# Performance work log

Measured on AMD Instinct MI355X. Metric: run time of the kernel, lower is better.

## Reference

```python
import jax, jax.numpy as jnp
import numpy as np

W_KERNEL = 5      # dilation kernel size (w)
K_BG = 0.1        # background weight (k)
RELAX = 5.0       # sigmoid temperature (relax)
INF = 1e4         # 'no zero in column' sentinel (>> image diagonal)
EPS = 1e-7        # DiceLoss eps


def setup_inputs() -> dict:
    key = jax.random.key(0)
    k1, k2 = jax.random.split(key)
    B, H, W = 32, 256, 256
    preds = jax.random.normal(k1, (B, H, W), dtype=jnp.float32)
    targets = (jax.random.uniform(k2, (B, H, W)) > 0.99).astype(jnp.float32)
    return {"preds": preds, "targets": targets}


def _dilate(t, w):
    # cv2.dilate with w x w ones kernel == sliding-window max, SAME padding
    pad = w // 2
    return jax.lax.reduce_window(t, -jnp.inf, jax.lax.max,
                                 (1, w, w), (1, 1, 1),
                                 [(0, 0), (pad, pad), (pad, pad)])


def _vertical_dist(zero_mask):
    # per-column distance (in rows) to nearest zero pixel; [B,H,W] -> [B,H,W]
    B, H, W = zero_mask.shape
    rows = jnp.moveaxis(zero_mask, 1, 0)  # [H,B,W]

    def step(carry, z):
        d = jnp.where(z, 0.0, jnp.minimum(carry + 1.0, INF))
        return d, d

    init = jnp.full((B, W), INF, dtype=jnp.float32)
    _, fwd = jax.lax.scan(step, init, rows)
    _, bwd = jax.lax.scan(step, init, rows[::-1])
    g = jnp.minimum(fwd, bwd[::-1])  # [H,B,W]
    return jnp.moveaxis(g, 0, 1)


def _edt(fat):
    # exact euclidean distance transform (distance to nearest zero pixel),
    # separable two-pass: vertical 1D distance, then horizontal min-plus.
    B, H, W = fat.shape
    g = _vertical_dist(fat == 0)  # [B,H,W]
    col = jnp.arange(W, dtype=jnp.float32)
    off2 = (col[:, None] - col[None, :]) ** 2  # [W_j, W_k]

    def per_img(gi):  # gi: [H,W]
        # d2[i,j] = min_k g[i,k]^2 + (j-k)^2   -> [H,W,W] intermediate
        d2 = jnp.min(gi[:, None, :] ** 2 + off2[None, :, :], axis=-1)
        return jnp.sqrt(d2)

    return jax.lax.map(per_img, g)  # sequential over batch caps memory


def _distance_maps(targets):
    fat = _dilate(targets, W_KERNEL)          # [B,H,W]
    d = _edt(fat)                              # [B,H,W]
    soft = jax.nn.sigmoid(d / RELAX)
    soft = soft - jnp.min(soft, axis=(1, 2), keepdims=True)
    mx = jnp.max(soft, axis=(1, 2), keepdims=True)
    soft = soft / jnp.where(mx > 0, mx, 1.0)
    dm_soft = soft + (1.0 - fat) * K_BG
    has_fg = jnp.max(targets, axis=(1, 2), keepdims=True) > 0
    return jnp.where(has_fg, dm_soft, 1.0 - targets)


def reference(preds, targets):
    p = jax.nn.sigmoid(preds)
    dm = jax.lax.stop_gradient(_distance_maps(targets))  # computed in numpy in torch => constant
    pw = p * dm
    bs = pw.shape[0]
    y_pred = pw.reshape(bs, 1, -1)
    y_true = targets.reshape(bs, 1, -1)
    # smp DiceLoss('binary', from_logits=False): dims=(0,2), smooth=0, eps=1e-7
    inter = jnp.sum(y_pred * y_true, axis=(0, 2))
    card = jnp.sum(y_pred + y_true, axis=(0, 2))
    dice = (2.0 * inter) / jnp.maximum(card, EPS)
    loss = 1.0 - dice
    mask = (jnp.sum(y_true, axis=(0, 2)) > 0).astype(loss.dtype)
    return jnp.mean(loss * mask)
```

## Files before the change

kernel.cpp:

```cpp
#include <hip/hip_runtime.h>
#include <math.h>

#define BB 32
#define HH 256
#define WW 256
#define HW (HH*WW)
#define K_BG 0.1f
#define RELAX 5.0f
#define EPS_D 1e-7
#define RPB 8

typedef unsigned long long u64;
typedef unsigned short u16;

__device__ __forceinline__ float sigf(float x) { return 1.0f / (1.0f + expf(-x)); }

__device__ __forceinline__ u64 shflx64(u64 x, int s) {
    return (u64)__shfl_xor((unsigned long long)x, s, 64);
}

__global__ void k_maskdil(const float* __restrict__ tg, u64* __restrict__ dmaskT,
                          u64* __restrict__ nzmask) {
    __shared__ u64 nz[20][4];
    __shared__ u64 hd[20][4];
    int blk = blockIdx.x;
    int b = blk >> 4, band = blk & 15;
    int r0 = band * 16;
    int t = threadIdx.x, w = t >> 6;
    const float* img = tg + b * HW;
    float v[20];
    #pragma unroll
    for (int rr = 0; rr < 20; ++rr) {
        int rg = r0 + rr - 2;
        v[rr] = (rg >= 0 && rg < HH) ? img[rg * WW + t] : 0.0f;
    }
    #pragma unroll
    for (int rr = 0; rr < 20; ++rr) {
        u64 bal = __ballot(v[rr] != 0.0f);
        if ((t & 63) == 0) nz[rr][w] = bal;
    }
    __syncthreads();
    if (t < 80) {
        int rr = t >> 2, k = t & 3;
        u64 m = nz[rr][k];
        u64 ml = (k > 0) ? nz[rr][k - 1] : 0ULL;
        u64 mr = (k < 3) ? nz[rr][k + 1] : 0ULL;
        hd[rr][k] = m | (m << 1) | (m << 2) | (m >> 1) | (m >> 2)
                  | (ml >> 62) | (ml >> 63) | (mr << 62) | (mr << 63);
    }
    if (t < 64) {
        int rr = t >> 2, k = t & 3;
        nzmask[b * 1024 + (r0 + rr) * 4 + k] = nz[rr + 2][k];
    }
    __syncthreads();
    if (t < 64) {
        int rr = t >> 2, k = t & 3;
        u64 o = hd[rr][k] | hd[rr + 1][k] | hd[rr + 2][k] | hd[rr + 3][k] | hd[rr + 4][k];
        dmaskT[b * 1024 + k * 256 + (r0 + rr)] = o;
    }
}

__global__ void k_transp(const u64* __restrict__ dmaskT, u64* __restrict__ cmask) {
    int b = blockIdx.x;
    int tid = threadIdx.x, lane = tid & 63, wv = tid >> 6;
    const u64* base = dmaskT + b * 1024;
    const u64 L32 = 0x00000000FFFFFFFFULL, L16 = 0x0000FFFF0000FFFFULL,
              L8  = 0x00FF00FF00FF00FFULL, L4  = 0x0F0F0F0F0F0F0F0FULL,
              L2  = 0x3333333333333333ULL, L1  = 0x5555555555555555ULL;
    #pragma unroll
    for (int w = 0; w < 4; ++w) {
        u64 x = base[w * 256 + wv * 64 + lane];
        u64 pp;
        pp = shflx64(x, 32); x = (lane & 32) ? ((x & ~L32) | ((pp & ~L32) >> 32)) : ((x & L32) | ((pp & L32) << 32));
        pp = shflx64(x, 16); x = (lane & 16) ? ((x & ~L16) | ((pp & ~L16) >> 16)) : ((x & L16) | ((pp & L16) << 16));
        pp = shflx64(x,  8); x = (lane &  8) ? ((x & ~L8 ) | ((pp & ~L8 ) >>  8)) : ((x & L8 ) | ((pp & L8 ) <<  8));
        pp = shflx64(x,  4); x = (lane &  4) ? ((x & ~L4 ) | ((pp & ~L4 ) >>  4)) : ((x & L4 ) | ((pp & L4 ) <<  4));
        pp = shflx64(x,  2); x = (lane &  2) ? ((x & ~L2 ) | ((pp & ~L2 ) >>  2)) : ((x & L2 ) | ((pp & L2 ) <<  2));
        pp = shflx64(x,  1); x = (lane &  1) ? ((x & ~L1 ) | ((pp & ~L1 ) >>  1)) : ((x & L1 ) | ((pp & L1 ) <<  1));
        cmask[b * 1024 + (w * 64 + lane) * 4 + wv] = x;
    }
}

__global__ __launch_bounds__(256) void k_mega(const float* __restrict__ preds,
                                              const u64* __restrict__ cmask,
                                              const u64* __restrict__ nzmask,
                                              float4* __restrict__ part1,
                                              float4* __restrict__ part2) {
    __shared__ u16 gS[RPB][WW];
    __shared__ float red[8][4];
    int blk = blockIdx.x;
    int b = blk >> 5, q = blk & 31;
    int i0 = q * RPB;
    int tid = threadIdx.x;
    int lane = tid & 63, wv = tid >> 6;
    int j = tid;

    float p[RPB];
    #pragma unroll
    for (int rr = 0; rr < RPB; ++rr)
        p[rr] = preds[(b * HH + i0 + rr) * WW + j];
    u64 nzw[RPB];
    #pragma unroll
    for (int rr = 0; rr < RPB; ++rr)
        nzw[rr] = nzmask[b * 1024 + (i0 + rr) * 4 + wv];

    u64 yw[4];
    {
        const u64* cm = cmask + b * 1024 + j * 4;
        #pragma unroll
        for (int g = 0; g < 4; ++g) yw[g] = ~cm[g];
    }

    int g0v[RPB], fgv[RPB];
    #pragma unroll
    for (int rr = 0; rr < RPB; ++rr) {
        int i = i0 + rr;
        int iw = i >> 6, ib = i & 63;
        u64 lowm  = (2ULL << ib) - 1ULL;
        u64 highm = ~((1ULL << ib) - 1ULL);
        int pu = -1, pd = -1;
        #pragma unroll
        for (int w = 0; w < 4; ++w) {
            u64 m = (w < iw) ? ~0ULL : ((w == iw) ? lowm : 0ULL);
            u64 z = yw[w] & m;
            int cand = (w << 6) + 63 - __clzll(z);
            pu = z ? cand : pu;
        }
        #pragma unroll
        for (int w = 3; w >= 0; --w) {
            u64 m = (w > iw) ? ~0ULL : ((w == iw) ? highm : 0ULL);
            u64 z = yw[w] & m;
            int cand = (w << 6) + (__ffsll((unsigned long long)z) - 1);
            pd = z ? cand : pd;
        }
        int up = (pu >= 0) ? (i - pu) : 10000;
        int dn = (pd >= 0) ? (pd - i) : 10000;
        int g0 = min(min(up, dn), 10000);
        g0v[rr] = g0;
        fgv[rr] = (int)((~yw[iw] >> ib) & 1ULL);
        gS[rr][j] = (u16)g0;
    }
    __syncthreads();

    float vals[8];
    #pragma unroll
    for (int qq = 0; qq < 6; ++qq) vals[qq] = 0.0f;
    vals[6] = 1e30f; vals[7] = 0.0f;
    #pragma unroll
    for (int rr = 0; rr < RPB; ++rr) {
        float gv = (float)g0v[rr];
        float best = gv * gv;
        #pragma unroll
        for (int r = 1; r <= 8; ++r) {
            float rf = (float)(r * r);
            int jl = j - r, jr = j + r;
            float vl = (jl >= 0) ? (float)gS[rr][jl] : 1e4f;
            float vr = (jr < WW) ? (float)gS[rr][jr] : 1e4f;
            best = fminf(best, fminf(fmaf(vl, vl, rf), fmaf(vr, vr, rf)));
        }
        for (int r = 9; r < WW; ++r) {
            float rf = (float)(r * r);
            if (rf >= best) break;
            int jl = j - r, jr = j + r;
            if (jl >= 0) { float v = (float)gS[rr][jl]; best = fminf(best, fmaf(v, v, rf)); }
            if (jr < WW) { float v = (float)gS[rr][jr]; best = fminf(best, fmaf(v, v, rf)); }
        }
        float dv = sqrtf(best);
        float sp = sigf(p[rr]);
        float sd = sigf(dv / RELAX);
        float tv = (float)((nzw[rr] >> (j & 63)) & 1ULL);
        vals[0] += sp * sd * tv;
        vals[1] += sp * tv;
        vals[2] += sp * sd;
        vals[3] += sp;
        vals[4] += fgv[rr] ? 0.0f : sp;
        vals[5] += tv;
        vals[6] = fminf(vals[6], dv);
        vals[7] = fmaxf(vals[7], dv);
    }
    for (int off = 32; off > 0; off >>= 1) {
        #pragma unroll
        for (int qq = 0; qq < 6; ++qq) vals[qq] += __shfl_down(vals[qq], off, 64);
        vals[6] = fminf(vals[6], __shfl_down(vals[6], off, 64));
        vals[7] = fmaxf(vals[7], __shfl_down(vals[7], off, 64));
    }
    if (lane == 0) {
        #pragma unroll
        for (int qq = 0; qq < 8; ++qq) red[qq][wv] = vals[qq];
    }
    __syncthreads();
    if (tid == 0) {
        float s[8];
        #pragma unroll
        for (int qq = 0; qq < 6; ++qq) s[qq] = red[qq][0] + red[qq][1] + red[qq][2] + red[qq][3];
        s[6] = fminf(fminf(red[6][0], red[6][1]), fminf(red[6][2], red[6][3]));
        s[7] = fmaxf(fmaxf(red[7][0], red[7][1]), fmaxf(red[7][2], red[7][3]));
        part1[blk] = make_float4(s[0], s[1], s[2], s[3]);
        part2[blk] = make_float4(s[4], s[5], s[6], s[7]);
    }
}

__global__ void k_tail(const float4* __restrict__ part1, const float4* __restrict__ part2,
                       float* __restrict__ out) {
    __shared__ float sI[32], sC[32], sA[32];
    int t = threadIdx.x;
    #pragma unroll
    for (int pass = 0; pass < 4; ++pass) {
        int img = pass * 8 + (t >> 5);
        int k = t & 31;
        float4 p1 = part1[img * 32 + k];
        float4 p2 = part2[img * 32 + k];
        float vals[8] = {p1.x, p1.y, p1.z, p1.w, p2.x, p2.y, p2.z, p2.w};
        for (int off = 16; off > 0; off >>= 1) {
            #pragma unroll
            for (int qq = 0; qq < 6; ++qq) vals[qq] += __shfl_down(vals[qq], off, 32);
            vals[6] = fminf(vals[6], __shfl_down(vals[6], off, 32));
            vals[7] = fmaxf(vals[7], __shfl_down(vals[7], off, 32));
        }
        if (k == 0) {
            float A = vals[0], Bs = vals[1], Ap = vals[2], Bp = vals[3];
            float Cp = vals[4], T = vals[5], dmn = vals[6], dmx = vals[7];
            float inter, card, any;
            if (dmx > 0.0f) {
                float smin = sigf(dmn / RELAX);
                float smax = sigf(dmx / RELAX);
                float m = smax - smin;
                float denom = (m > 0.0f) ? m : 1.0f;
                inter = (A - smin * Bs) / denom;
                card  = (Ap - smin * Bp) / denom + K_BG * Cp + T;
                any = 1.0f;
            } else {
                inter = 0.0f;
                card = Bp - Bs + T;
                any = 0.0f;
            }
            sI[img] = inter; sC[img] = card; sA[img] = any;
        }
    }
    __syncthreads();
    if (t == 0) {
        double I = 0.0, C = 0.0;
        int any = 0;
        for (int b = 0; b < BB; ++b) {
            I += (double)sI[b]; C += (double)sC[b];
            any |= (sA[b] > 0.0f);
        }
        double dice = 2.0 * I / fmax(C, (double)EPS_D);
        out[0] = any ? (float)(1.0 - dice) : 0.0f;
    }
}

extern "C" void kernel_launch(void* const* d_in, const int* in_sizes, int n_in,
                              void* d_out, int out_size, void* d_ws, size_t ws_size,
                              hipStream_t stream) {
    const float* preds = (const float*)d_in[0];
    const float* tg    = (const float*)d_in[1];
    float* out = (float*)d_out;

    u64* dmaskT   = (u64*)d_ws;
    u64* nzmask   = dmaskT + BB * 1024;
    u64* cmask    = nzmask + BB * 1024;
    float4* part1 = (float4*)(cmask + BB * 1024);
    float4* part2 = part1 + BB * 32;

    hipLaunchKernelGGL(k_maskdil, dim3(BB * 16), dim3(WW), 0, stream, tg, dmaskT, nzmask);
    hipLaunchKernelGGL(k_transp, dim3(BB), dim3(WW), 0, stream, dmaskT, cmask);
    hipLaunchKernelGGL(k_mega, dim3(BB * 32), dim3(WW), 0, stream, preds, cmask, nzmask,
                       part1, part2);
    hipLaunchKernelGGL(k_tail, dim3(1), dim3(256), 0, stream, part1, part2, out);
}
```

Before: 93.02 us.

## Fuse bit-transpose into main kernel and unroll horizontal EDT search by 8

```diff
diff --git a/kernel.cpp b/kernel.cpp
--- a/kernel.cpp
+++ b/kernel.cpp
@@ -60,9 +60,30 @@
     }
 }
 
-__global__ void k_transp(const u64* __restrict__ dmaskT, u64* __restrict__ cmask) {
-    int b = blockIdx.x;
-    int tid = threadIdx.x, lane = tid & 63, wv = tid >> 6;
+__global__ __launch_bounds__(256) void k_mega(const float* __restrict__ preds,
+                                              const u64* __restrict__ dmaskT,
+                                              const u64* __restrict__ nzmask,
+                                              float4* __restrict__ part1,
+                                              float4* __restrict__ part2) {
+    __shared__ u64 colT[4 * 256];
+    __shared__ u16 gS[RPB][WW];
+    __shared__ float red[8][4];
+    int blk = blockIdx.x;
+    int b = blk >> 5, q = blk & 31;
+    int i0 = q * RPB;
+    int tid = threadIdx.x;
+    int lane = tid & 63, wv = tid >> 6;
+    int j = tid;
+
+    float p[RPB];
+    #pragma unroll
+    for (int rr = 0; rr < RPB; ++rr)
+        p[rr] = preds[(b * HH + i0 + rr) * WW + j];
+    u64 nzw[RPB];
+    #pragma unroll
+    for (int rr = 0; rr < RPB; ++rr)
+        nzw[rr] = nzmask[b * 1024 + (i0 + rr) * 4 + wv];
+
     const u64* base = dmaskT + b * 1024;
     const u64 L32 = 0x00000000FFFFFFFFULL, L16 = 0x0000FFFF0000FFFFULL,
               L8  = 0x00FF00FF00FF00FFULL, L4  = 0x0F0F0F0F0F0F0F0FULL,
@@ -77,39 +98,13 @@
         pp = shflx64(x,  4); x = (lane &  4) ? ((x & ~L4 ) | ((pp & ~L4 ) >>  4)) : ((x & L4 ) | ((pp & L4 ) <<  4));
         pp = shflx64(x,  2); x = (lane &  2) ? ((x & ~L2 ) | ((pp & ~L2 ) >>  2)) : ((x & L2 ) | ((pp & L2 ) <<  2));
         pp = shflx64(x,  1); x = (lane &  1) ? ((x & ~L1 ) | ((pp & ~L1 ) >>  1)) : ((x & L1 ) | ((pp & L1 ) <<  1));
-        cmask[b * 1024 + (w * 64 + lane) * 4 + wv] = x;
-    }
-}
-
-__global__ __launch_bounds__(256) void k_mega(const float* __restrict__ preds,
-                                              const u64* __restrict__ cmask,
-                                              const u64* __restrict__ nzmask,
-                                              float4* __restrict__ part1,
-                                              float4* __restrict__ part2) {
-    __shared__ u16 gS[RPB][WW];
-    __shared__ float red[8][4];
-    int blk = blockIdx.x;
-    int b = blk >> 5, q = blk & 31;
-    int i0 = q * RPB;
-    int tid = threadIdx.x;
-    int lane = tid & 63, wv = tid >> 6;
-    int j = tid;
-
-    float p[RPB];
-    #pragma unroll
-    for (int rr = 0; rr < RPB; ++rr)
-        p[rr] = preds[(b * HH + i0 + rr) * WW + j];
-    u64 nzw[RPB];
-    #pragma unroll
-    for (int rr = 0; rr < RPB; ++rr)
-        nzw[rr] = nzmask[b * 1024 + (i0 + rr) * 4 + wv];
+        colT[wv * 256 + w * 64 + lane] = x;
+    }
+    __syncthreads();
 
     u64 yw[4];
-    {
-        const u64* cm = cmask + b * 1024 + j * 4;
-        #pragma unroll
-        for (int g = 0; g < 4; ++g) yw[g] = ~cm[g];
-    }
+    #pragma unroll
+    for (int g = 0; g < 4; ++g) yw[g] = ~colT[g * 256 + j];
 
     int g0v[RPB], fgv[RPB];
     #pragma unroll
@@ -158,12 +153,17 @@
             float vr = (jr < WW) ? (float)gS[rr][jr] : 1e4f;
             best = fminf(best, fminf(fmaf(vl, vl, rf), fmaf(vr, vr, rf)));
         }
-        for (int r = 9; r < WW; ++r) {
-            float rf = (float)(r * r);
-            if (rf >= best) break;
-            int jl = j - r, jr = j + r;
-            if (jl >= 0) { float v = (float)gS[rr][jl]; best = fminf(best, fmaf(v, v, rf)); }
-            if (jr < WW) { float v = (float)gS[rr][jr]; best = fminf(best, fmaf(v, v, rf)); }
+        for (int rc = 9; rc < WW + 8; rc += 8) {
+            if ((float)(rc * rc) >= best) break;
+            #pragma unroll
+            for (int dr = 0; dr < 8; ++dr) {
+                int r = rc + dr;
+                float rf = (float)(r * r);
+                int jl = j - r, jr = j + r;
+                float vl = (jl >= 0) ? (float)gS[rr][jl] : 1e4f;
+                float vr = (jr < WW) ? (float)gS[rr][jr] : 1e4f;
+                best = fminf(best, fminf(fmaf(vl, vl, rf), fmaf(vr, vr, rf)));
+            }
         }
         float dv = sqrtf(best);
         float sp = sigf(p[rr]);
@@ -259,13 +259,11 @@
 
     u64* dmaskT   = (u64*)d_ws;
     u64* nzmask   = dmaskT + BB * 1024;
-    u64* cmask    = nzmask + BB * 1024;
-    float4* part1 = (float4*)(cmask + BB * 1024);
+    float4* part1 = (float4*)(nzmask + BB * 1024);
     float4* part2 = part1 + BB * 32;
 
     hipLaunchKernelGGL(k_maskdil, dim3(BB * 16), dim3(WW), 0, stream, tg, dmaskT, nzmask);
-    hipLaunchKernelGGL(k_transp, dim3(BB), dim3(WW), 0, stream, dmaskT, cmask);
-    hipLaunchKernelGGL(k_mega, dim3(BB * 32), dim3(WW), 0, stream, preds, cmask, nzmask,
+    hipLaunchKernelGGL(k_mega, dim3(BB * 32), dim3(WW), 0, stream, preds, dmaskT, nzmask,
                        part1, part2);
     hipLaunchKernelGGL(k_tail, dim3(1), dim3(256), 0, stream, part1, part2, out);
 }
```

Measured after the change: 90.82 us. -2.4%, faster.
